# Performance work log

Measured on AMD Instinct MI355X. Metric: run time of the kernel, lower is better.

The kernel has to match this reference:

```python
import jax, jax.numpy as jnp
import numpy as np

B, N, ND, ED, HD = 2, 384, 128, 32, 128
MSG_IN = 2 * ND + ED + 1  # 289
LN_EPS = 1e-3  # keras LayerNormalization default epsilon


def setup_inputs() -> dict:
    key = jax.random.key(0)
    ks = jax.random.split(key, 20)
    s = 0.05
    return {
        "h": jax.random.normal(ks[0], (B, N, ND), jnp.float32),
        "x": jax.random.normal(ks[1], (B, N, 3), jnp.float32),
        "edge_attr": jax.random.normal(ks[2], (B, N, N, ED), jnp.float32),
        "atom_mask": jnp.ones((B, N), jnp.float32),
        "msg_w1": jax.random.normal(ks[3], (MSG_IN, HD), jnp.float32) * s,
        "msg_b1": jnp.zeros((HD,), jnp.float32),
        "msg_w2": jax.random.normal(ks[4], (HD, HD), jnp.float32) * s,
        "msg_b2": jnp.zeros((HD,), jnp.float32),
        "node_w1": jax.random.normal(ks[5], (ND + HD, HD), jnp.float32) * s,
        "node_b1": jnp.zeros((HD,), jnp.float32),
        "node_w2": jax.random.normal(ks[6], (HD, ND), jnp.float32) * s,
        "node_b2": jnp.zeros((ND,), jnp.float32),
        "coord_w1": jax.random.normal(ks[7], (HD, HD), jnp.float32) * s,
        "coord_b1": jnp.zeros((HD,), jnp.float32),
        "coord_w2": jax.random.normal(ks[8], (HD, 1), jnp.float32) * 0.01,  # RandomNormal(0, 0.01)
        "ln_gamma": jnp.ones((ND,), jnp.float32),
        "ln_beta": jnp.zeros((ND,), jnp.float32),
        "adj": jax.random.randint(ks[9], (B, N, N), 0, 2, jnp.int32),
    }


def _layernorm(y, gamma, beta):
    mu = jnp.mean(y, axis=-1, keepdims=True)
    var = jnp.mean(jnp.square(y - mu), axis=-1, keepdims=True)
    return (y - mu) * jax.lax.rsqrt(var + LN_EPS) * gamma + beta


def reference(h, x, edge_attr, atom_mask,
              msg_w1, msg_b1, msg_w2, msg_b2,
              node_w1, node_b1, node_w2, node_b2,
              coord_w1, coord_b1, coord_w2,
              ln_gamma, ln_beta, adj):
    n = h.shape[1]
    rel_pos = x[:, :, None, :] - x[:, None, :, :]              # [B,N,N,3]
    dist_sq = jnp.sum(rel_pos ** 2, axis=-1, keepdims=True)    # [B,N,N,1]
    h_i = jnp.broadcast_to(h[:, :, None, :], (h.shape[0], n, n, h.shape[-1]))
    h_j = jnp.broadcast_to(h[:, None, :, :], (h.shape[0], n, n, h.shape[-1]))
    msg_in = jnp.concatenate([h_i, h_j, edge_attr, dist_sq], axis=-1)  # [B,N,N,289]
    m = jax.nn.silu(msg_in @ msg_w1 + msg_b1)
    m = jax.nn.silu(m @ msg_w2 + msg_b2)                        # [B,N,N,HD]
    adj_f = adj.astype(m.dtype)[..., None]                      # [B,N,N,1]
    m = m * adj_f
    h_agg = jnp.sum(m, axis=2)                                  # [B,N,HD]
    u = jax.nn.silu(jnp.concatenate([h, h_agg], axis=-1) @ node_w1 + node_b1)
    h_update = u @ node_w2 + node_b2
    h_new = _layernorm(h + h_update, ln_gamma, ln_beta)
    # coordinate update
    cw = jax.nn.silu(m @ coord_w1 + coord_b1) @ coord_w2        # [B,N,N,1]
    dist = jnp.sqrt(dist_sq + 1e-8)
    cw = cw / (dist + 1.0) * adj_f
    x_agg = jnp.sum(cw * rel_pos, axis=2) * atom_mask[..., None]
    x_new = x + x_agg
    return (h_new, x_new)
```

## Files before the change

### kernel.cpp

```cpp
#include <hip/hip_runtime.h>

typedef float f32x4 __attribute__((ext_vector_type(4)));
typedef unsigned int u32x4 __attribute__((ext_vector_type(4)));
typedef unsigned int u32x2 __attribute__((ext_vector_type(2)));
typedef __bf16 bf16x8 __attribute__((ext_vector_type(8)));

#define LDS_WET   0
#define LDS_W2T   8192
#define LDS_WC1T  40960
#define LDS_ACTW  73728
#define LDS_FP    108544
#define LDS_CIDX  111616
#define LDS_WCNT  112384
#define LDS_BYTES 112452

__device__ __forceinline__ unsigned short f2bf(float f) {
  unsigned int u = __builtin_bit_cast(unsigned int, f);
  unsigned int r = u + 0x7FFFu + ((u >> 16) & 1u);
  return (unsigned short)(r >> 16);
}
__device__ __forceinline__ unsigned int pk2(float lo, float hi) {
  unsigned short a = __builtin_bit_cast(unsigned short, (__bf16)lo);
  unsigned short b = __builtin_bit_cast(unsigned short, (__bf16)hi);
  return (unsigned int)a | ((unsigned int)b << 16);
}
__device__ __forceinline__ float bflo(unsigned int u) {
  return __builtin_bit_cast(float, u << 16);
}
__device__ __forceinline__ float bfhi(unsigned int u) {
  return __builtin_bit_cast(float, u & 0xFFFF0000u);
}
__device__ __forceinline__ float silu_f(float xv) {
  float t = __builtin_amdgcn_exp2f(-1.44269504088896f * xv);
  return xv * __builtin_amdgcn_rcpf(1.0f + t);
}
__device__ __forceinline__ f32x4 mfma16(u32x4 a, u32x4 b, f32x4 c) {
  return __builtin_amdgcn_mfma_f32_16x16x32_bf16(
      __builtin_bit_cast(bf16x8, a), __builtin_bit_cast(bf16x8, b), c, 0, 0, 0);
}
__device__ __forceinline__ void gload_lds16(const void* g, void* l) {
  __builtin_amdgcn_global_load_lds(
      (const __attribute__((address_space(1))) unsigned int*)g,
      (__attribute__((address_space(3))) unsigned int*)l, 16, 0, 0);
}

__global__ void egnn_pre(const float* __restrict__ h,
                         const float* __restrict__ msg_w1,
                         const float* __restrict__ msg_b1,
                         float* __restrict__ his,
                         unsigned short* __restrict__ hjw) {
  __shared__ float hr[128];
  const int row = blockIdx.x;
  const int t = threadIdx.x;
  if (t < 128) hr[t] = h[(size_t)row*128 + t];
  __syncthreads();
  const int col = t & 127;
  const int base = (t < 128) ? 0 : 128;
  float s = (t < 128) ? msg_b1[col] : 0.0f;
  #pragma unroll 4
  for (int k = 0; k < 128; ++k) s += hr[k] * msg_w1[(size_t)(base + k)*128 + col];
  if (t < 128) his[(size_t)row*128 + col] = s;
  else         hjw[(size_t)row*128 + col] = f2bf(s);
}

__global__ void egnn_wpack(const float* __restrict__ msg_w1,
                           const float* __restrict__ msg_w2,
                           const float* __restrict__ coord_w1,
                           unsigned short* __restrict__ weP,
                           unsigned short* __restrict__ w2P,
                           unsigned short* __restrict__ wc1P) {
  const int idx = blockIdx.x*256 + threadIdx.x;
  if (idx < 32*128) {
    int d = idx >> 5, k = idx & 31;
    weP[idx] = f2bf(msg_w1[(size_t)(256 + k)*128 + d]);
  }
  if (idx < 128*128) {
    int d = idx >> 7, k = (idx & 127) ^ ((d & 7) << 3);
    w2P[idx]  = f2bf(msg_w2[(size_t)k*128 + d]);
    wc1P[idx] = f2bf(coord_w1[(size_t)k*128 + d]);
  }
}

__launch_bounds__(512, 1)
__global__ void egnn_main(
    const float* __restrict__ h, const float* __restrict__ x,
    const float* __restrict__ eattr, const float* __restrict__ amask,
    const float* __restrict__ msg_w1, const float* __restrict__ msg_b2,
    const float* __restrict__ node_w1, const float* __restrict__ node_b1,
    const float* __restrict__ node_w2, const float* __restrict__ node_b2,
    const float* __restrict__ coord_b1, const float* __restrict__ coord_w2,
    const float* __restrict__ ln_g, const float* __restrict__ ln_b,
    const int* __restrict__ adj, const float* __restrict__ his,
    const unsigned short* __restrict__ hjw,
    const unsigned short* __restrict__ weP,
    const unsigned short* __restrict__ w2P,
    const unsigned short* __restrict__ wc1P,
    float* __restrict__ out)
{
  extern __shared__ char smem[];
  short* weT  = (short*)(smem + LDS_WET);
  short* w2T  = (short*)(smem + LDS_W2T);
  short* wc1T = (short*)(smem + LDS_WC1T);
  float* fp   = (float*)(smem + LDS_FP);
  float* HisL = fp;          float* wdL  = fp + 128;
  float* b2L  = fp + 256;    float* bc1L = fp + 384;
  float* wc2L = fp + 512;    float* hrow = fp + 640;
  unsigned short* cidx16 = (unsigned short*)(smem + LDS_CIDX);
  int* wcnt = (int*)(smem + LDS_WCNT);
  int* wsc  = wcnt + 8;

  const int tid  = threadIdx.x;
  const int bi   = blockIdx.x;
  const int bb   = (bi / 384) * 384;
  const int wave = tid >> 6;
  const int lane = tid & 63;
  const int g    = lane >> 4;
  const int lr   = lane & 15;
  const int swz  = (lr & 7) << 3;
  short* actW = (short*)(smem + LDS_ACTW) + wave*(16*136);

  const bool pred = (tid < 384) && (adj[(size_t)bi*384 + tid] != 0);
  const unsigned long long bmask = __ballot(pred);
  if (lane == 0) wcnt[wave] = __popcll(bmask);

  {
    const int t16 = tid * 16;
    gload_lds16((const char*)weP + t16, smem + LDS_WET + t16);
    #pragma unroll
    for (int it = 0; it < 4; ++it) {
      gload_lds16((const char*)w2P  + it*8192 + t16, smem + LDS_W2T  + it*8192 + t16);
      gload_lds16((const char*)wc1P + it*8192 + t16, smem + LDS_WC1T + it*8192 + t16);
    }
  }
  if (tid < 128) {
    HisL[tid] = his[(size_t)bi*128 + tid];
    wdL[tid]  = msg_w1[288*128 + tid];
    b2L[tid]  = msg_b2[tid];
    bc1L[tid] = coord_b1[tid];
    wc2L[tid] = coord_w2[tid];
    hrow[tid] = h[(size_t)bi*128 + tid];
  }
  __syncthreads();

  u32x4 awf[8];
  #pragma unroll
  for (int cf = 0; cf < 8; ++cf)
    awf[cf] = *(const u32x4*)(weT + (cf*16 + lr)*32 + g*8);

  if (tid == 0) {
    int run = 0;
    #pragma unroll
    for (int w = 0; w < 8; ++w) { wsc[w] = run; run += wcnt[w]; }
    wsc[8] = run;
  }
  __syncthreads();
  if (pred) {
    int rank = __popcll(bmask & ((1ull << lane) - 1ull));
    cidx16[wsc[wave] + rank] = (unsigned short)tid;
  }
  const int deg = wsc[8];
  const float xi0 = x[bi*3+0], xi1 = x[bi*3+1], xi2 = x[bi*3+2];
  f32x4 hacc2[8];
  #pragma unroll
  for (int cf = 0; cf < 8; ++cf) hacc2[cf] = (f32x4){0.f, 0.f, 0.f, 0.f};
  float xc0 = 0.0f, xc1 = 0.0f, xc2 = 0.0f;
  __syncthreads();

  const int nchunk = (deg + 127) >> 7;
  for (int ch = 0; ch < nchunk; ++ch) {
    const int sbase = ch*128 + wave*16;
    if (sbase >= deg) continue;
    const int s = sbase + lr;
    const bool valid = (s < deg);
    const int cj = valid ? (int)cidx16[s] : 0;
    const float vm = valid ? 1.0f : 0.0f;
    const float* xp = x + (size_t)(bb + cj)*3;
    const float r0 = xi0 - xp[0], r1 = xi1 - xp[1], r2 = xi2 - xp[2];
    const float dq = r0*r0 + r1*r1 + r2*r2;
    const float fc = __builtin_amdgcn_rcpf(sqrtf(dq + 1e-8f) + 1.0f) * vm;
    const float c0 = fc*r0, c1 = fc*r1, c2 = fc*r2;
    const float* ep = eattr + ((size_t)bi*384 + cj)*32 + g*8;
    const float4 p0 = ((const float4*)ep)[0];
    const float4 p1 = ((const float4*)ep)[1];
    const u32x4 be = (u32x4){pk2(p0.x, p0.y), pk2(p0.z, p0.w),
                             pk2(p1.x, p1.y), pk2(p1.z, p1.w)};

    __builtin_amdgcn_s_setprio(1);

    #pragma unroll
    for (int cf = 0; cf < 8; ++cf) {
      const int dO = cf*16 + 4*g;
      u32x2 hj = *(const u32x2*)(hjw + (size_t)(bb + cj)*128 + dO);
      f32x4 hv = *(const f32x4*)(HisL + dO);
      f32x4 wv = *(const f32x4*)(wdL + dO);
      f32x4 acc;
      acc[0] = hv[0] + dq*wv[0] + bflo(hj[0]);
      acc[1] = hv[1] + dq*wv[1] + bfhi(hj[0]);
      acc[2] = hv[2] + dq*wv[2] + bflo(hj[1]);
      acc[3] = hv[3] + dq*wv[3] + bfhi(hj[1]);
      acc = mfma16(awf[cf], be, acc);
      *(u32x2*)(actW + lr*136 + dO) =
          (u32x2){pk2(silu_f(acc[0]), silu_f(acc[1])),
                  pk2(silu_f(acc[2]), silu_f(acc[3]))};
    }

    u32x4 bk[4];
    #pragma unroll
    for (int kk = 0; kk < 4; ++kk)
      bk[kk] = *(const u32x4*)(actW + lr*136 + kk*32 + g*8);
    #pragma unroll
    for (int cf = 0; cf < 8; ++cf) {
      const int dO = cf*16 + 4*g;
      f32x4 a = *(const f32x4*)(b2L + dO);
      #pragma unroll
      for (int kk = 0; kk < 4; ++kk) {
        u32x4 aw2 = *(const u32x4*)(w2T + (((cf*16 + lr)*128 + kk*32 + g*8) ^ swz));
        a = mfma16(aw2, bk[kk], a);
      }
      float v0 = silu_f(a[0]) * vm, v1 = silu_f(a[1]) * vm;
      float v2 = silu_f(a[2]) * vm, v3 = silu_f(a[3]) * vm;
      hacc2[cf][0] += v0; hacc2[cf][1] += v1;
      hacc2[cf][2] += v2; hacc2[cf][3] += v3;
      *(u32x2*)(actW + lr*136 + dO) = (u32x2){pk2(v0, v1), pk2(v2, v3)};
    }

    u32x4 bm[4];
    #pragma unroll
    for (int kk = 0; kk < 4; ++kk)
      bm[kk] = *(const u32x4*)(actW + lr*136 + kk*32 + g*8);
    float cwp = 0.0f;
    #pragma unroll
    for (int cf = 0; cf < 8; ++cf) {
      const int dO = cf*16 + 4*g;
      f32x4 a = *(const f32x4*)(bc1L + dO);
      #pragma unroll
      for (int kk = 0; kk < 4; ++kk) {
        u32x4 aw3 = *(const u32x4*)(wc1T + (((cf*16 + lr)*128 + kk*32 + g*8) ^ swz));
        a = mfma16(aw3, bm[kk], a);
      }
      f32x4 wv = *(const f32x4*)(wc2L + dO);
      cwp += silu_f(a[0])*wv[0] + silu_f(a[1])*wv[1]
           + silu_f(a[2])*wv[2] + silu_f(a[3])*wv[3];
    }
    __builtin_amdgcn_s_setprio(0);
    cwp += __shfl_xor(cwp, 16, 64);
    cwp += __shfl_xor(cwp, 32, 64);
    if (lane < 16) { xc0 += cwp*c0; xc1 += cwp*c1; xc2 += cwp*c2; }
  }

  __syncthreads();
  #pragma unroll
  for (int cf = 0; cf < 8; ++cf) {
    #pragma unroll
    for (int r = 0; r < 4; ++r) {
      float v = hacc2[cf][r];
      v += __shfl_xor(v, 1, 64); v += __shfl_xor(v, 2, 64);
      v += __shfl_xor(v, 4, 64); v += __shfl_xor(v, 8, 64);
      hacc2[cf][r] = v;
    }
  }
  float* actF  = (float*)(smem + LDS_ACTW);
  float* hpart = actF;
  float* xcf   = actF + 1024;
  float* red   = actF + 1408;
  float* hagg  = actF + 1920;
  float* uvec  = actF + 2048;
  float* lnr   = actF + 2176;
  if (lr == 0) {
    #pragma unroll
    for (int cf = 0; cf < 8; ++cf)
      #pragma unroll
      for (int r = 0; r < 4; ++r)
        hpart[wave*128 + cf*16 + 4*g + r] = hacc2[cf][r];
  }
  if (lane < 16) {
    const int idx = wave*16 + lr;
    xcf[idx] = xc0; xcf[128 + idx] = xc1; xcf[256 + idx] = xc2;
  }
  __syncthreads();
  if (tid < 128) {
    float s = 0.0f;
    #pragma unroll
    for (int w = 0; w < 8; ++w) s += hpart[w*128 + tid];
    hagg[tid] = s;
  }
  if (tid < 3) {
    float sx = 0.0f;
    #pragma unroll 8
    for (int j = 0; j < 128; ++j) sx += xcf[tid*128 + j];
    out[98304 + (size_t)bi*3 + tid] = x[bi*3 + tid] + sx * amask[bi];
  }
  __syncthreads();

  {
    const int d = tid & 127, q = tid >> 7;
    float s = 0.0f;
    for (int k = q*64; k < q*64 + 64; ++k) {
      const float inv = (k < 128) ? hrow[k] : hagg[k - 128];
      s += inv * node_w1[(size_t)k*128 + d];
    }
    red[q*128 + d] = s;
  }
  __syncthreads();
  if (tid < 128)
    uvec[tid] = silu_f(red[tid] + red[128+tid] + red[256+tid] + red[384+tid] + node_b1[tid]);
  __syncthreads();

  {
    const int d = tid & 127, q = tid >> 7;
    float s = 0.0f;
    for (int k = q*32; k < q*32 + 32; ++k) s += uvec[k] * node_w2[(size_t)k*128 + d];
    red[q*128 + d] = s;
  }
  __syncthreads();
  float y = 0.0f;
  if (tid < 128)
    y = hrow[tid] + red[tid] + red[128+tid] + red[256+tid] + red[384+tid] + node_b2[tid];

  float ssum = (tid < 128) ? y : 0.0f;
  #pragma unroll
  for (int mm = 1; mm < 64; mm <<= 1) ssum += __shfl_xor(ssum, mm, 64);
  if (tid < 128 && lane == 0) lnr[wave] = ssum;
  __syncthreads();
  const float mu = (lnr[0] + lnr[1]) * (1.0f/128.0f);
  float yc = (tid < 128) ? (y - mu) : 0.0f;
  float sq = yc * yc;
  #pragma unroll
  for (int mm = 1; mm < 64; mm <<= 1) sq += __shfl_xor(sq, mm, 64);
  if (tid < 128 && lane == 0) lnr[2 + wave] = sq;
  __syncthreads();
  if (tid < 128) {
    const float var = (lnr[2] + lnr[3]) * (1.0f/128.0f);
    out[(size_t)bi*128 + tid] = yc * rsqrtf(var + 1e-3f) * ln_g[tid] + ln_b[tid];
  }
}

extern "C" void kernel_launch(void* const* d_in, const int* in_sizes, int n_in,
                              void* d_out, int out_size, void* d_ws, size_t ws_size,
                              hipStream_t stream) {
  const float* h        = (const float*)d_in[0];
  const float* x        = (const float*)d_in[1];
  const float* eattr    = (const float*)d_in[2];
  const float* amask    = (const float*)d_in[3];
  const float* msg_w1   = (const float*)d_in[4];
  const float* msg_b1   = (const float*)d_in[5];
  const float* msg_w2   = (const float*)d_in[6];
  const float* msg_b2   = (const float*)d_in[7];
  const float* node_w1  = (const float*)d_in[8];
  const float* node_b1  = (const float*)d_in[9];
  const float* node_w2  = (const float*)d_in[10];
  const float* node_b2  = (const float*)d_in[11];
  const float* coord_w1 = (const float*)d_in[12];
  const float* coord_b1 = (const float*)d_in[13];
  const float* coord_w2 = (const float*)d_in[14];
  const float* ln_g     = (const float*)d_in[15];
  const float* ln_b     = (const float*)d_in[16];
  const int*   adj      = (const int*)d_in[17];
  float* out = (float*)d_out;
  float* his = (float*)d_ws;
  unsigned short* hjw  = (unsigned short*)((char*)d_ws + 393216);
  unsigned short* weP  = (unsigned short*)((char*)d_ws + 589824);
  unsigned short* w2P  = (unsigned short*)((char*)d_ws + 598016);
  unsigned short* wc1P = (unsigned short*)((char*)d_ws + 630784);

  hipFuncSetAttribute((const void*)egnn_main,
                      hipFuncAttributeMaxDynamicSharedMemorySize, LDS_BYTES);

  egnn_pre<<<768, 256, 0, stream>>>(h, msg_w1, msg_b1, his, hjw);
  egnn_wpack<<<64, 256, 0, stream>>>(msg_w1, msg_w2, coord_w1, weP, w2P, wc1P);
  egnn_main<<<768, 512, LDS_BYTES, stream>>>(h, x, eattr, amask, msg_w1,
      msg_b2, node_w1, node_b1, node_w2, node_b2, coord_b1, coord_w2,
      ln_g, ln_b, adj, his, hjw, weP, w2P, wc1P, out);
}
```

Baseline: 79.34 us.

## Prefetch next chunk's neighbor state and merge weight-pack kernel into pre kernel

The main loop now issues the gather loads for the next 128-neighbor chunk (x, edge_attr, the hj bf16 rows) into a second register set before computing the current chunk, then swaps the sets at the end of the iteration. This is meant to hide global gather latency behind the three MFMA stages. Separately, the weight-packing kernel is folded into extra blocks of egnn_pre, removing one launch, and the pre kernel's unroll factor rises from 4 to 8. The doubled state raises register pressure in a kernel already running one block of 512 threads per CU.

```diff
diff --git a/kernel.cpp b/kernel.cpp
--- a/kernel.cpp
+++ b/kernel.cpp
@@ -47,9 +47,27 @@
 __global__ void egnn_pre(const float* __restrict__ h,
                          const float* __restrict__ msg_w1,
                          const float* __restrict__ msg_b1,
+                         const float* __restrict__ msg_w2,
+                         const float* __restrict__ coord_w1,
                          float* __restrict__ his,
-                         unsigned short* __restrict__ hjw) {
+                         unsigned short* __restrict__ hjw,
+                         unsigned short* __restrict__ weP,
+                         unsigned short* __restrict__ w2P,
+                         unsigned short* __restrict__ wc1P) {
   __shared__ float hr[128];
+  if (blockIdx.x >= 768) {
+    const int idx = (blockIdx.x - 768)*256 + threadIdx.x;
+    if (idx < 32*128) {
+      int d = idx >> 5, k = idx & 31;
+      weP[idx] = f2bf(msg_w1[(size_t)(256 + k)*128 + d]);
+    }
+    {
+      int d = idx >> 7, k = (idx & 127) ^ ((d & 7) << 3);
+      w2P[idx]  = f2bf(msg_w2[(size_t)k*128 + d]);
+      wc1P[idx] = f2bf(coord_w1[(size_t)k*128 + d]);
+    }
+    return;
+  }
   const int row = blockIdx.x;
   const int t = threadIdx.x;
   if (t < 128) hr[t] = h[(size_t)row*128 + t];
@@ -57,28 +75,10 @@
   const int col = t & 127;
   const int base = (t < 128) ? 0 : 128;
   float s = (t < 128) ? msg_b1[col] : 0.0f;
-  #pragma unroll 4
+  #pragma unroll 8
   for (int k = 0; k < 128; ++k) s += hr[k] * msg_w1[(size_t)(base + k)*128 + col];
   if (t < 128) his[(size_t)row*128 + col] = s;
   else         hjw[(size_t)row*128 + col] = f2bf(s);
-}
-
-__global__ void egnn_wpack(const float* __restrict__ msg_w1,
-                           const float* __restrict__ msg_w2,
-                           const float* __restrict__ coord_w1,
-                           unsigned short* __restrict__ weP,
-                           unsigned short* __restrict__ w2P,
-                           unsigned short* __restrict__ wc1P) {
-  const int idx = blockIdx.x*256 + threadIdx.x;
-  if (idx < 32*128) {
-    int d = idx >> 5, k = idx & 31;
-    weP[idx] = f2bf(msg_w1[(size_t)(256 + k)*128 + d]);
-  }
-  if (idx < 128*128) {
-    int d = idx >> 7, k = (idx & 127) ^ ((d & 7) << 3);
-    w2P[idx]  = f2bf(msg_w2[(size_t)k*128 + d]);
-    wc1P[idx] = f2bf(coord_w1[(size_t)k*128 + d]);
-  }
 }
 
 __launch_bounds__(512, 1)
@@ -166,39 +166,54 @@
   float xc0 = 0.0f, xc1 = 0.0f, xc2 = 0.0f;
   __syncthreads();
 
+  float dqA, vmA, c0A, c1A, c2A; u32x4 beA; u32x2 hjA[8];
+  float dqB, vmB, c0B, c1B, c2B; u32x4 beB; u32x2 hjB[8];
+
+#define LOAD_STATE(SFX, SIDX) do {                                         \
+    const int s_ = (SIDX);                                                 \
+    const bool valid_ = (s_ < deg);                                        \
+    const int cj_ = valid_ ? (int)cidx16[s_] : 0;                          \
+    vm##SFX = valid_ ? 1.0f : 0.0f;                                        \
+    const float* xp_ = x + (size_t)(bb + cj_)*3;                           \
+    const float r0_ = xi0 - xp_[0], r1_ = xi1 - xp_[1], r2_ = xi2 - xp_[2];\
+    dq##SFX = r0_*r0_ + r1_*r1_ + r2_*r2_;                                 \
+    const float fc_ = __builtin_amdgcn_rcpf(sqrtf(dq##SFX + 1e-8f) + 1.0f) \
+                      * vm##SFX;                                           \
+    c0##SFX = fc_*r0_; c1##SFX = fc_*r1_; c2##SFX = fc_*r2_;               \
+    const float* ep_ = eattr + ((size_t)bi*384 + cj_)*32 + g*8;            \
+    const float4 p0_ = ((const float4*)ep_)[0];                            \
+    const float4 p1_ = ((const float4*)ep_)[1];                            \
+    be##SFX = (u32x4){pk2(p0_.x, p0_.y), pk2(p0_.z, p0_.w),                \
+                      pk2(p1_.x, p1_.y), pk2(p1_.z, p1_.w)};               \
+    _Pragma("unroll")                                                      \
+    for (int cf_ = 0; cf_ < 8; ++cf_)                                      \
+      hj##SFX[cf_] = *(const u32x2*)(hjw + (size_t)(bb + cj_)*128          \
+                                     + cf_*16 + 4*g);                      \
+  } while (0)
+
   const int nchunk = (deg + 127) >> 7;
+  if (wave*16 < deg) LOAD_STATE(A, wave*16 + lr);
+
   for (int ch = 0; ch < nchunk; ++ch) {
     const int sbase = ch*128 + wave*16;
     if (sbase >= deg) continue;
-    const int s = sbase + lr;
-    const bool valid = (s < deg);
-    const int cj = valid ? (int)cidx16[s] : 0;
-    const float vm = valid ? 1.0f : 0.0f;
-    const float* xp = x + (size_t)(bb + cj)*3;
-    const float r0 = xi0 - xp[0], r1 = xi1 - xp[1], r2 = xi2 - xp[2];
-    const float dq = r0*r0 + r1*r1 + r2*r2;
-    const float fc = __builtin_amdgcn_rcpf(sqrtf(dq + 1e-8f) + 1.0f) * vm;
-    const float c0 = fc*r0, c1 = fc*r1, c2 = fc*r2;
-    const float* ep = eattr + ((size_t)bi*384 + cj)*32 + g*8;
-    const float4 p0 = ((const float4*)ep)[0];
-    const float4 p1 = ((const float4*)ep)[1];
-    const u32x4 be = (u32x4){pk2(p0.x, p0.y), pk2(p0.z, p0.w),
-                             pk2(p1.x, p1.y), pk2(p1.z, p1.w)};
+    const int nbase = sbase + 128;
+    const bool hasNext = (nbase < deg);
+    if (hasNext) LOAD_STATE(B, nbase + lr);
 
     __builtin_amdgcn_s_setprio(1);
 
     #pragma unroll
     for (int cf = 0; cf < 8; ++cf) {
       const int dO = cf*16 + 4*g;
-      u32x2 hj = *(const u32x2*)(hjw + (size_t)(bb + cj)*128 + dO);
       f32x4 hv = *(const f32x4*)(HisL + dO);
       f32x4 wv = *(const f32x4*)(wdL + dO);
       f32x4 acc;
-      acc[0] = hv[0] + dq*wv[0] + bflo(hj[0]);
-      acc[1] = hv[1] + dq*wv[1] + bfhi(hj[0]);
-      acc[2] = hv[2] + dq*wv[2] + bflo(hj[1]);
-      acc[3] = hv[3] + dq*wv[3] + bfhi(hj[1]);
-      acc = mfma16(awf[cf], be, acc);
+      acc[0] = hv[0] + dqA*wv[0] + bflo(hjA[cf][0]);
+      acc[1] = hv[1] + dqA*wv[1] + bfhi(hjA[cf][0]);
+      acc[2] = hv[2] + dqA*wv[2] + bflo(hjA[cf][1]);
+      acc[3] = hv[3] + dqA*wv[3] + bfhi(hjA[cf][1]);
+      acc = mfma16(awf[cf], beA, acc);
       *(u32x2*)(actW + lr*136 + dO) =
           (u32x2){pk2(silu_f(acc[0]), silu_f(acc[1])),
                   pk2(silu_f(acc[2]), silu_f(acc[3]))};
@@ -217,8 +232,8 @@
         u32x4 aw2 = *(const u32x4*)(w2T + (((cf*16 + lr)*128 + kk*32 + g*8) ^ swz));
         a = mfma16(aw2, bk[kk], a);
       }
-      float v0 = silu_f(a[0]) * vm, v1 = silu_f(a[1]) * vm;
-      float v2 = silu_f(a[2]) * vm, v3 = silu_f(a[3]) * vm;
+      float v0 = silu_f(a[0]) * vmA, v1 = silu_f(a[1]) * vmA;
+      float v2 = silu_f(a[2]) * vmA, v3 = silu_f(a[3]) * vmA;
       hacc2[cf][0] += v0; hacc2[cf][1] += v1;
       hacc2[cf][2] += v2; hacc2[cf][3] += v3;
       *(u32x2*)(actW + lr*136 + dO) = (u32x2){pk2(v0, v1), pk2(v2, v3)};
@@ -245,8 +260,15 @@
     __builtin_amdgcn_s_setprio(0);
     cwp += __shfl_xor(cwp, 16, 64);
     cwp += __shfl_xor(cwp, 32, 64);
-    if (lane < 16) { xc0 += cwp*c0; xc1 += cwp*c1; xc2 += cwp*c2; }
-  }
+    if (lane < 16) { xc0 += cwp*c0A; xc1 += cwp*c1A; xc2 += cwp*c2A; }
+
+    if (hasNext) {
+      dqA = dqB; vmA = vmB; c0A = c0B; c1A = c1B; c2A = c2B; beA = beB;
+      #pragma unroll
+      for (int cf = 0; cf < 8; ++cf) hjA[cf] = hjB[cf];
+    }
+  }
+#undef LOAD_STATE
 
   __syncthreads();
   #pragma unroll
@@ -366,8 +388,8 @@
   hipFuncSetAttribute((const void*)egnn_main,
                       hipFuncAttributeMaxDynamicSharedMemorySize, LDS_BYTES);
 
-  egnn_pre<<<768, 256, 0, stream>>>(h, msg_w1, msg_b1, his, hjw);
-  egnn_wpack<<<64, 256, 0, stream>>>(msg_w1, msg_w2, coord_w1, weP, w2P, wc1P);
+  egnn_pre<<<832, 256, 0, stream>>>(h, msg_w1, msg_b1, msg_w2, coord_w1,
+                                    his, hjw, weP, w2P, wc1P);
   egnn_main<<<768, 512, LDS_BYTES, stream>>>(h, x, eattr, amask, msg_w1,
       msg_b2, node_w1, node_b1, node_w2, node_b2, coord_b1, coord_w2,
       ln_g, ln_b, adj, his, hjw, weP, w2P, wc1P, out);
```

Result: slower. 92.43 us (+16.5%).
